# Optimization experiments

Measured on AMD Instinct MI355X. Metric: run time of the kernel, lower is better.

## Reference

```python
import jax, jax.numpy as jnp
import numpy as np
from jax import lax

B, D, N, C = 8, 1, 12288, 256
H = 8            # num_heads
WS = 64          # window size (pixels per window)
HID = 1024       # mlp hidden = 4*C
K = 9            # conv kernel size
EPS = 1e-5


def setup_inputs() -> dict:
    key = jax.random.key(0)
    ks = jax.random.split(key, 8)
    w = lambda i, shape: jax.random.normal(ks[i], shape, jnp.float32) * 0.02
    return {
        "x": jax.random.normal(ks[0], (B, D, N, C), jnp.float32),
        "ln1_g": jnp.ones((C,), jnp.float32),
        "ln1_b": jnp.zeros((C,), jnp.float32),
        "conv_w": w(1, (C, C, K)),            # OIH layout (out_ch, in_ch, k)
        "conv_b": jnp.zeros((C,), jnp.float32),
        "qkv_w": w(2, (C, 3 * C)),            # stored (in, out): y = x @ W + b
        "qkv_b": jnp.zeros((3 * C,), jnp.float32),
        "proj_w": w(3, (C, C)),
        "proj_b": jnp.zeros((C,), jnp.float32),
        "ln2_g": jnp.ones((C,), jnp.float32),
        "ln2_b": jnp.zeros((C,), jnp.float32),
        "fc1_w": w(4, (C, HID)),
        "fc1_b": jnp.zeros((HID,), jnp.float32),
        "fc2_w": w(5, (HID, C)),
        "fc2_b": jnp.zeros((C,), jnp.float32),
    }


def _layernorm(x, g, b):
    mu = jnp.mean(x, axis=-1, keepdims=True)
    var = jnp.mean(jnp.square(x - mu), axis=-1, keepdims=True)
    return (x - mu) * lax.rsqrt(var + EPS) * g + b


def reference(x, ln1_g, ln1_b, conv_w, conv_b, qkv_w, qkv_b,
              proj_w, proj_b, ln2_g, ln2_b, fc1_w, fc1_b, fc2_w, fc2_b):
    shortcut = x                                  # (B, D, N, C)
    h = _layernorm(x, ln1_g, ln1_b)

    # Conv1d over pixel dim N, channels C, same padding
    hc = h.reshape(B * D, N, C).transpose(0, 2, 1)            # (BD, C, N)
    hc = lax.conv_general_dilated(
        hc, conv_w, window_strides=(1,), padding=[((K - 1) // 2, (K - 1) // 2)],
        dimension_numbers=("NCH", "OIH", "NCH"))
    hc = hc + conv_b[None, :, None]
    h = hc.transpose(0, 2, 1).reshape(B, D, N, C)

    # Window partition (no shift): (B*D*N/WS, WS, C)
    win = h.reshape(-1, WS, C)
    hd = C // H
    qkv = (win @ qkv_w + qkv_b).reshape(-1, WS, 3, H, hd)
    q = qkv[:, :, 0].transpose(0, 2, 1, 3)        # (nW, H, WS, hd)
    k = qkv[:, :, 1].transpose(0, 2, 1, 3)
    v = qkv[:, :, 2].transpose(0, 2, 1, 3)
    scale = hd ** (-0.5)
    attn = jnp.einsum("whqd,whkd->whqk", q * scale, k)
    attn = jax.nn.softmax(attn, axis=-1)
    out = jnp.einsum("whqk,whkd->whqd", attn, v)
    out = out.transpose(0, 2, 1, 3).reshape(-1, WS, C)
    out = out @ proj_w + proj_b

    h = out.reshape(B, D, N, C)
    x1 = shortcut + h                             # residual 1
    mlp_in = _layernorm(x1, ln2_g, ln2_b)
    mlp = jax.nn.gelu(mlp_in @ fc1_w + fc1_b, approximate=False) @ fc2_w + fc2_b
    return x1 + mlp                               # residual 2
```

## Files before the change

kernel.cpp:

```cpp
#include <hip/hip_runtime.h>

#define DEVI __device__ __forceinline__

typedef __attribute__((ext_vector_type(4))) float  f32x4;
typedef __attribute__((ext_vector_type(8))) short  s16x8;
typedef __attribute__((ext_vector_type(4))) short  s16x4;
typedef __attribute__((ext_vector_type(8))) __bf16 bf16x8;

constexpr int  Cc  = 256;
constexpr int  Nn  = 12288;
constexpr int  NP  = 12296;
constexpr long TOK = 98304;

DEVI short f2bf(float f) {
  unsigned u = __builtin_bit_cast(unsigned, f);
  u += 0x7fffu + ((u >> 16) & 1u);
  return (short)(u >> 16);
}

DEVI f32x4 MFMA(s16x8 a, s16x8 b, f32x4 c) {
  return __builtin_amdgcn_mfma_f32_16x16x32_bf16(
      __builtin_bit_cast(bf16x8, a), __builtin_bit_cast(bf16x8, b), c, 0, 0, 0);
}

DEVI void gld16(const void* g, void* l) {
  __builtin_amdgcn_global_load_lds(
      (const __attribute__((address_space(1))) void*)g,
      (__attribute__((address_space(3))) void*)l, 16, 0, 0);
}

DEVI void stage_tile(const short* __restrict__ base, long row0, int ld, int k0,
                     short (*dst)[32], int w, int lane) {
#pragma unroll
  for (int c = 0; c < 2; ++c) {
    int s = w * 2 + c;
    const short* g = base + (row0 + s * 16 + (lane >> 2)) * (long)ld + k0 + (lane & 3) * 8;
    gld16(g, &dst[s * 16][0]);
  }
}

__global__ void prep_k(const float* __restrict__ qkv_w, const float* __restrict__ proj_w,
                       const float* __restrict__ fc1_w, const float* __restrict__ fc2_w,
                       const float* __restrict__ conv_w,
                       short* __restrict__ qkvWt, short* __restrict__ projWt,
                       short* __restrict__ fc1Wt, short* __restrict__ fc2Wt,
                       short* __restrict__ convWt, short* __restrict__ hp) {
  int idx = blockIdx.x * 256 + threadIdx.x;
  if (idx < 196608) {
    int o = idx >> 8, i = idx & 255;
    qkvWt[idx] = f2bf(qkv_w[i * 768 + o]);
    return;
  }
  idx -= 196608;
  if (idx < 65536) {
    int o = idx >> 8, i = idx & 255;
    projWt[idx] = f2bf(proj_w[i * 256 + o]);
    return;
  }
  idx -= 65536;
  if (idx < 262144) {
    int o = idx >> 8, i = idx & 255;
    fc1Wt[idx] = f2bf(fc1_w[i * 1024 + o]);
    return;
  }
  idx -= 262144;
  if (idx < 262144) {
    int o = idx >> 10, i = idx & 1023;
    fc2Wt[idx] = f2bf(fc2_w[i * 256 + o]);
    return;
  }
  idx -= 262144;
  if (idx < 589824) {
    int k = idx >> 16, co = (idx >> 8) & 255, ci = idx & 255;
    convWt[idx] = f2bf(conv_w[co * 2304 + ci * 9 + k]);
    return;
  }
  idx -= 589824;
  if (idx < 16384) {
    int b = idx >> 11, rem = idx & 2047;
    int rs = rem >> 8, ch = rem & 255;
    int p = rs < 4 ? rs : 12288 + rs;
    hp[((long)b * NP + p) * 256 + ch] = 0;
  }
}

__global__ __launch_bounds__(256) void ln_k(const float* __restrict__ x,
                                            const float* __restrict__ gw,
                                            const float* __restrict__ bw,
                                            short* __restrict__ out, int pad) {
  const int tid = threadIdx.x, w = tid >> 6, lane = tid & 63;
  const long t = (long)blockIdx.x * 4 + w;
  f32x4 v = *((const f32x4*)(x + t * 256) + lane);
  float s  = v[0] + v[1] + v[2] + v[3];
  float ss = v[0] * v[0] + v[1] * v[1] + v[2] * v[2] + v[3] * v[3];
#pragma unroll
  for (int mk = 1; mk < 64; mk <<= 1) {
    s  += __shfl_xor(s, mk);
    ss += __shfl_xor(ss, mk);
  }
  const float mu   = s * (1.0f / 256.0f);
  const float var  = ss * (1.0f / 256.0f) - mu * mu;
  const float rstd = rsqrtf(var + 1e-5f);
  f32x4 g4 = *((const f32x4*)gw + lane);
  f32x4 b4 = *((const f32x4*)bw + lane);
  const long orow = pad ? (t + (t / Nn) * 8 + 4) : t;
  s16x4 o4;
#pragma unroll
  for (int j = 0; j < 4; ++j) o4[j] = f2bf((v[j] - mu) * rstd * g4[j] + b4[j]);
  *((s16x4*)(out + orow * 256) + lane) = o4;
}

template <int EPI>
__global__ __launch_bounds__(256, 2) void gemm_k(
    const short* __restrict__ A, int lda,
    const short* __restrict__ Bt,
    const float* __restrict__ bias,
    const float* res, short* outS, float* outF,
    int ldo, int K) {
  __shared__ __align__(16) short As[128][32];
  __shared__ __align__(16) short Bs[128][32];
  const int tid = threadIdx.x, w = tid >> 6, lane = tid & 63;
  const int q = lane >> 4, r16 = lane & 15;
  const long row0 = (long)blockIdx.y * 128;
  const int  col0 = blockIdx.x * 128;
  const int  wr = w >> 1, wc = w & 1;
  f32x4 acc[4][4] = {};

  for (int k0 = 0; k0 < K; k0 += 32) {
    stage_tile(A, row0, lda, k0, As, w, lane);
    stage_tile(Bt, col0, K, k0, Bs, w, lane);
    __syncthreads();
    s16x8 af[4], bfv[4];
#pragma unroll
    for (int m = 0; m < 4; ++m) af[m] = *(const s16x8*)&As[wr * 64 + m * 16 + r16][q * 8];
#pragma unroll
    for (int n = 0; n < 4; ++n) bfv[n] = *(const s16x8*)&Bs[wc * 64 + n * 16 + r16][q * 8];
#pragma unroll
    for (int m = 0; m < 4; ++m)
#pragma unroll
      for (int n = 0; n < 4; ++n) acc[m][n] = MFMA(af[m], bfv[n], acc[m][n]);
    __syncthreads();
  }

  const long orow = row0 + wr * 64;
  const int  ocol = col0 + wc * 64;
#pragma unroll
  for (int n = 0; n < 4; ++n) {
    const int   gc = ocol + n * 16 + r16;
    const float bn = bias[gc];
#pragma unroll
    for (int m = 0; m < 4; ++m) {
      const long gr = orow + m * 16 + q * 4;
#pragma unroll
      for (int r = 0; r < 4; ++r) {
        float v = acc[m][n][r] + bn;
        const long o = (gr + r) * (long)ldo + gc;
        if constexpr (EPI == 0) {
          outS[o] = f2bf(v);
        } else if constexpr (EPI == 1) {
          outF[o] = v + res[o];
        } else {
          float t = 0.5f * v * (1.0f + erff(v * 0.70710678118654752f));
          outS[o] = f2bf(t);
        }
      }
    }
  }
}

__global__ __launch_bounds__(256, 2) void conv_k(const short* __restrict__ hp,
                                                 const short* __restrict__ convWt,
                                                 const float* __restrict__ bias,
                                                 short* __restrict__ out) {
  __shared__ __align__(16) short As[128][32];
  __shared__ __align__(16) short Bs[128][32];
  const int tid = threadIdx.x, w = tid >> 6, lane = tid & 63;
  const int q = lane >> 4, r16 = lane & 15;
  const long row0 = (long)blockIdx.y * 128;
  const int  col0 = blockIdx.x * 128;
  const int  b  = (int)(row0 / Nn);
  const int  n0 = (int)(row0 % Nn);
  const long hpbase = (long)b * NP + n0;
  const int  wr = w >> 1, wc = w & 1;
  f32x4 acc[4][4] = {};

  for (int k = 0; k < 9; ++k) {
    const short* Ak = hp + (hpbase + k) * 256;
    const short* Bk = convWt + k * 65536;
    for (int k0 = 0; k0 < 256; k0 += 32) {
      stage_tile(Ak, 0, 256, k0, As, w, lane);
      stage_tile(Bk, col0, 256, k0, Bs, w, lane);
      __syncthreads();
      s16x8 af[4], bfv[4];
#pragma unroll
      for (int m = 0; m < 4; ++m) af[m] = *(const s16x8*)&As[wr * 64 + m * 16 + r16][q * 8];
#pragma unroll
      for (int n = 0; n < 4; ++n) bfv[n] = *(const s16x8*)&Bs[wc * 64 + n * 16 + r16][q * 8];
#pragma unroll
      for (int m = 0; m < 4; ++m)
#pragma unroll
        for (int n = 0; n < 4; ++n) acc[m][n] = MFMA(af[m], bfv[n], acc[m][n]);
      __syncthreads();
    }
  }

  const long orow = row0 + wr * 64;
  const int  ocol = col0 + wc * 64;
#pragma unroll
  for (int n = 0; n < 4; ++n) {
    const int   gc = ocol + n * 16 + r16;
    const float bn = bias[gc];
#pragma unroll
    for (int m = 0; m < 4; ++m) {
      const long gr = orow + m * 16 + q * 4;
#pragma unroll
      for (int r = 0; r < 4; ++r) out[(gr + r) * 256L + gc] = f2bf(acc[m][n][r] + bn);
    }
  }
}

__global__ __launch_bounds__(256, 2) void attn_k(const short* __restrict__ qkv,
                                                 short* __restrict__ o) {
  __shared__ __align__(16) short Pt[4][64][68];
  __shared__ __align__(16) short Vs[4][64][32];
  const int tid = threadIdx.x, w = tid >> 6, lane = tid & 63;
  const int q = lane >> 4, r16 = lane & 15;
  const int job = blockIdx.x * 4 + w;
  const int win = job >> 3, h = job & 7;
  const short* base = qkv + (long)win * 64 * 768;

#pragma unroll
  for (int c = 0; c < 4; ++c) {
    const int idx16 = c * 64 + lane;
    const short* g = base + (long)(idx16 >> 2) * 768 + 512 + h * 32 + (idx16 & 3) * 8;
    gld16(g, (char*)&Vs[w][0][0] + c * 1024);
  }

  s16x8 aq[4], bk[4];
#pragma unroll
  for (int m = 0; m < 4; ++m)
    aq[m] = *(const s16x8*)(base + (long)(m * 16 + r16) * 768 + h * 32 + q * 8);
#pragma unroll
  for (int n = 0; n < 4; ++n)
    bk[n] = *(const s16x8*)(base + (long)(n * 16 + r16) * 768 + 256 + h * 32 + q * 8);
  f32x4 sc[4][4] = {};
#pragma unroll
  for (int m = 0; m < 4; ++m)
#pragma unroll
    for (int n = 0; n < 4; ++n) sc[m][n] = MFMA(aq[m], bk[n], sc[m][n]);

  const float scale = 0.17677669529663687f;
#pragma unroll
  for (int m = 0; m < 4; ++m) {
#pragma unroll
    for (int r = 0; r < 4; ++r) {
      float a0 = sc[m][0][r] * scale, a1 = sc[m][1][r] * scale;
      float a2 = sc[m][2][r] * scale, a3 = sc[m][3][r] * scale;
      float mx = fmaxf(fmaxf(a0, a1), fmaxf(a2, a3));
      mx = fmaxf(mx, __shfl_xor(mx, 1));
      mx = fmaxf(mx, __shfl_xor(mx, 2));
      mx = fmaxf(mx, __shfl_xor(mx, 4));
      mx = fmaxf(mx, __shfl_xor(mx, 8));
      float e0 = __expf(a0 - mx), e1 = __expf(a1 - mx);
      float e2 = __expf(a2 - mx), e3 = __expf(a3 - mx);
      float sm = e0 + e1 + e2 + e3;
      sm += __shfl_xor(sm, 1);
      sm += __shfl_xor(sm, 2);
      sm += __shfl_xor(sm, 4);
      sm += __shfl_xor(sm, 8);
      float inv = 1.0f / sm;
      sc[m][0][r] = e0 * inv; sc[m][1][r] = e1 * inv;
      sc[m][2][r] = e2 * inv; sc[m][3][r] = e3 * inv;
    }
  }

#pragma unroll
  for (int m = 0; m < 4; ++m)
#pragma unroll
    for (int n = 0; n < 4; ++n) {
      s16x4 p4;
#pragma unroll
      for (int r = 0; r < 4; ++r) p4[r] = f2bf(sc[m][n][r]);
      *(s16x4*)&Pt[w][n * 16 + r16][m * 16 + q * 4] = p4;
    }

  asm volatile("s_waitcnt vmcnt(0)" ::: "memory");

  f32x4 oa[4][2] = {};
#pragma unroll
  for (int ks = 0; ks < 2; ++ks) {
    s16x8 bv[2];
#pragma unroll
    for (int nt = 0; nt < 2; ++nt)
#pragma unroll
      for (int jj = 0; jj < 8; ++jj)
        bv[nt][jj] = Vs[w][ks * 32 + q * 8 + jj][nt * 16 + r16];
#pragma unroll
    for (int m = 0; m < 4; ++m) {
      s16x8 ap;
#pragma unroll
      for (int jj = 0; jj < 8; ++jj)
        ap[jj] = Pt[w][ks * 32 + q * 8 + jj][m * 16 + r16];
#pragma unroll
      for (int nt = 0; nt < 2; ++nt) oa[m][nt] = MFMA(ap, bv[nt], oa[m][nt]);
    }
  }

  short* ob = o + (long)win * 64 * 256 + h * 32;
#pragma unroll
  for (int m = 0; m < 4; ++m)
#pragma unroll
    for (int nt = 0; nt < 2; ++nt)
#pragma unroll
      for (int r = 0; r < 4; ++r)
        ob[(long)(m * 16 + q * 4 + r) * 256 + nt * 16 + r16] = f2bf(oa[m][nt][r]);
}

extern "C" void kernel_launch(void* const* d_in, const int* in_sizes, int n_in,
                              void* d_out, int out_size, void* d_ws, size_t ws_size,
                              hipStream_t stream) {
  const float* x      = (const float*)d_in[0];
  const float* ln1_g  = (const float*)d_in[1];
  const float* ln1_b  = (const float*)d_in[2];
  const float* conv_w = (const float*)d_in[3];
  const float* conv_b = (const float*)d_in[4];
  const float* qkv_w  = (const float*)d_in[5];
  const float* qkv_b  = (const float*)d_in[6];
  const float* proj_w = (const float*)d_in[7];
  const float* proj_b = (const float*)d_in[8];
  const float* ln2_g  = (const float*)d_in[9];
  const float* ln2_b  = (const float*)d_in[10];
  const float* fc1_w  = (const float*)d_in[11];
  const float* fc1_b  = (const float*)d_in[12];
  const float* fc2_w  = (const float*)d_in[13];
  const float* fc2_b  = (const float*)d_in[14];
  float* out = (float*)d_out;

  constexpr long HPsz = (long)8 * NP * 256;
  constexpr long Qsz  = TOK * 768;
  constexpr long Csz  = TOK * 256;
  short* ws    = (short*)d_ws;
  short* hp    = ws;
  short* qkvB  = ws + HPsz;
  short* cvB   = ws + HPsz + Qsz;
  short* hidB  = qkvB;
  short* wts   = ws + HPsz + Qsz + Csz;
  short* qkvWt  = wts;
  short* projWt = qkvWt + 196608;
  short* fc1Wt  = projWt + 65536;
  short* fc2Wt  = fc1Wt + 262144;
  short* convWt = fc2Wt + 262144;

  prep_k<<<5440, 256, 0, stream>>>(qkv_w, proj_w, fc1_w, fc2_w, conv_w,
                                   qkvWt, projWt, fc1Wt, fc2Wt, convWt, hp);
  ln_k<<<24576, 256, 0, stream>>>(x, ln1_g, ln1_b, hp, 1);
  conv_k<<<dim3(2, 768), 256, 0, stream>>>(hp, convWt, conv_b, cvB);
  gemm_k<0><<<dim3(6, 768), 256, 0, stream>>>(cvB, 256, qkvWt, qkv_b,
                                              nullptr, qkvB, nullptr, 768, 256);
  attn_k<<<3072, 256, 0, stream>>>(qkvB, hp);
  gemm_k<1><<<dim3(2, 768), 256, 0, stream>>>(hp, 256, projWt, proj_b,
                                              x, nullptr, out, 256, 256);
  ln_k<<<24576, 256, 0, stream>>>(out, ln2_g, ln2_b, hp, 0);
  gemm_k<2><<<dim3(8, 768), 256, 0, stream>>>(hp, 256, fc1Wt, fc1_b,
                                              nullptr, hidB, nullptr, 1024, 256);
  gemm_k<1><<<dim3(2, 768), 256, 0, stream>>>(hidB, 1024, fc2Wt, fc2_b,
                                              out, nullptr, out, 256, 1024);
}
```

Measured before the change: 740.8 us.

## Reuse conv input tile across taps, widen GEMM K-tiles, fuse proj with LN2

Measured after the change: 671.3 us. 9.4% less time.

```diff
diff --git a/kernel.cpp b/kernel.cpp
--- a/kernel.cpp
+++ b/kernel.cpp
@@ -7,7 +7,6 @@
 typedef __attribute__((ext_vector_type(4))) short  s16x4;
 typedef __attribute__((ext_vector_type(8))) __bf16 bf16x8;
 
-constexpr int  Cc  = 256;
 constexpr int  Nn  = 12288;
 constexpr int  NP  = 12296;
 constexpr long TOK = 98304;
@@ -29,14 +28,23 @@
       (__attribute__((address_space(3))) void*)l, 16, 0, 0);
 }
 
-DEVI void stage_tile(const short* __restrict__ base, long row0, int ld, int k0,
-                     short (*dst)[32], int w, int lane) {
-#pragma unroll
-  for (int c = 0; c < 2; ++c) {
-    int s = w * 2 + c;
-    const short* g = base + (row0 + s * 16 + (lane >> 2)) * (long)ld + k0 + (lane & 3) * 8;
-    gld16(g, &dst[s * 16][0]);
-  }
+template <int UNITS>
+DEVI void stage64(const short* __restrict__ g_base, long g_row0, int ld, int k0,
+                  short* __restrict__ lds, int w, int lane) {
+#pragma unroll
+  for (int cc = 0; cc < UNITS; ++cc) {
+    const int u = cc * 256 + w * 64 + lane;
+    const int row = u >> 3, ch = u & 7;
+    const short* g = g_base + (g_row0 + row) * (long)ld + k0 + ch * 8;
+    gld16(g, lds + (cc * 256 + w * 64) * 8);
+  }
+}
+
+DEVI void xcd_decode(int W, int total, int ncol, long& row0, int& col0) {
+  const int per = total >> 3;
+  const int L = (W & 7) * per + (W >> 3);
+  row0 = (long)(L / ncol) * 128;
+  col0 = (L % ncol) * 128;
 }
 
 __global__ void prep_k(const float* __restrict__ qkv_w, const float* __restrict__ proj_w,
@@ -71,7 +79,8 @@
   }
   idx -= 262144;
   if (idx < 589824) {
-    int k = idx >> 16, co = (idx >> 8) & 255, ci = idx & 255;
+    int co = idx / 2304, rem = idx % 2304;
+    int k = rem >> 8, ci = rem & 255;
     convWt[idx] = f2bf(conv_w[co * 2304 + ci * 9 + k]);
     return;
   }
@@ -87,7 +96,7 @@
 __global__ __launch_bounds__(256) void ln_k(const float* __restrict__ x,
                                             const float* __restrict__ gw,
                                             const float* __restrict__ bw,
-                                            short* __restrict__ out, int pad) {
+                                            short* __restrict__ out) {
   const int tid = threadIdx.x, w = tid >> 6, lane = tid & 63;
   const long t = (long)blockIdx.x * 4 + w;
   f32x4 v = *((const f32x4*)(x + t * 256) + lane);
@@ -103,7 +112,7 @@
   const float rstd = rsqrtf(var + 1e-5f);
   f32x4 g4 = *((const f32x4*)gw + lane);
   f32x4 b4 = *((const f32x4*)bw + lane);
-  const long orow = pad ? (t + (t / Nn) * 8 + 4) : t;
+  const long orow = t + (t / Nn) * 8 + 4;
   s16x4 o4;
 #pragma unroll
   for (int j = 0; j < 4; ++j) o4[j] = f2bf((v[j] - mu) * rstd * g4[j] + b4[j]);
@@ -116,29 +125,32 @@
     const short* __restrict__ Bt,
     const float* __restrict__ bias,
     const float* res, short* outS, float* outF,
-    int ldo, int K) {
-  __shared__ __align__(16) short As[128][32];
-  __shared__ __align__(16) short Bs[128][32];
+    int ldo, int K, int ncol) {
+  __shared__ __align__(16) short As[128][64];
+  __shared__ __align__(16) short Bs[128][64];
   const int tid = threadIdx.x, w = tid >> 6, lane = tid & 63;
   const int q = lane >> 4, r16 = lane & 15;
-  const long row0 = (long)blockIdx.y * 128;
-  const int  col0 = blockIdx.x * 128;
-  const int  wr = w >> 1, wc = w & 1;
+  long row0; int col0;
+  xcd_decode(blockIdx.x, gridDim.x, ncol, row0, col0);
+  const int wr = w >> 1, wc = w & 1;
   f32x4 acc[4][4] = {};
 
-  for (int k0 = 0; k0 < K; k0 += 32) {
-    stage_tile(A, row0, lda, k0, As, w, lane);
-    stage_tile(Bt, col0, K, k0, Bs, w, lane);
+  for (int k0 = 0; k0 < K; k0 += 64) {
+    stage64<4>(A, row0, lda, k0, &As[0][0], w, lane);
+    stage64<4>(Bt, col0, K, k0, &Bs[0][0], w, lane);
     __syncthreads();
-    s16x8 af[4], bfv[4];
-#pragma unroll
-    for (int m = 0; m < 4; ++m) af[m] = *(const s16x8*)&As[wr * 64 + m * 16 + r16][q * 8];
-#pragma unroll
-    for (int n = 0; n < 4; ++n) bfv[n] = *(const s16x8*)&Bs[wc * 64 + n * 16 + r16][q * 8];
-#pragma unroll
-    for (int m = 0; m < 4; ++m)
-#pragma unroll
-      for (int n = 0; n < 4; ++n) acc[m][n] = MFMA(af[m], bfv[n], acc[m][n]);
+#pragma unroll
+    for (int kk = 0; kk < 2; ++kk) {
+      s16x8 af[4], bfv[4];
+#pragma unroll
+      for (int m = 0; m < 4; ++m) af[m] = *(const s16x8*)&As[wr * 64 + m * 16 + r16][kk * 32 + q * 8];
+#pragma unroll
+      for (int n = 0; n < 4; ++n) bfv[n] = *(const s16x8*)&Bs[wc * 64 + n * 16 + r16][kk * 32 + q * 8];
+#pragma unroll
+      for (int m = 0; m < 4; ++m)
+#pragma unroll
+        for (int n = 0; n < 4; ++n) acc[m][n] = MFMA(af[m], bfv[n], acc[m][n]);
+    }
     __syncthreads();
   }
 
@@ -172,34 +184,37 @@
                                                  const short* __restrict__ convWt,
                                                  const float* __restrict__ bias,
                                                  short* __restrict__ out) {
-  __shared__ __align__(16) short As[128][32];
-  __shared__ __align__(16) short Bs[128][32];
+  __shared__ __align__(16) short As[160][64];
+  __shared__ __align__(16) short Bs[128][64];
   const int tid = threadIdx.x, w = tid >> 6, lane = tid & 63;
   const int q = lane >> 4, r16 = lane & 15;
-  const long row0 = (long)blockIdx.y * 128;
-  const int  col0 = blockIdx.x * 128;
+  long row0; int col0;
+  xcd_decode(blockIdx.x, gridDim.x, 2, row0, col0);
   const int  b  = (int)(row0 / Nn);
   const int  n0 = (int)(row0 % Nn);
-  const long hpbase = (long)b * NP + n0;
+  const long abase = (long)b * NP + n0;
   const int  wr = w >> 1, wc = w & 1;
   f32x4 acc[4][4] = {};
 
-  for (int k = 0; k < 9; ++k) {
-    const short* Ak = hp + (hpbase + k) * 256;
-    const short* Bk = convWt + k * 65536;
-    for (int k0 = 0; k0 < 256; k0 += 32) {
-      stage_tile(Ak, 0, 256, k0, As, w, lane);
-      stage_tile(Bk, col0, 256, k0, Bs, w, lane);
+  for (int k0 = 0; k0 < 256; k0 += 64) {
+    stage64<5>(hp, abase, 256, k0, &As[0][0], w, lane);
+    for (int tap = 0; tap < 9; ++tap) {
+      stage64<4>(convWt, col0, 2304, tap * 256 + k0, &Bs[0][0], w, lane);
       __syncthreads();
-      s16x8 af[4], bfv[4];
-#pragma unroll
-      for (int m = 0; m < 4; ++m) af[m] = *(const s16x8*)&As[wr * 64 + m * 16 + r16][q * 8];
-#pragma unroll
-      for (int n = 0; n < 4; ++n) bfv[n] = *(const s16x8*)&Bs[wc * 64 + n * 16 + r16][q * 8];
-#pragma unroll
-      for (int m = 0; m < 4; ++m)
-#pragma unroll
-        for (int n = 0; n < 4; ++n) acc[m][n] = MFMA(af[m], bfv[n], acc[m][n]);
+#pragma unroll
+      for (int kk = 0; kk < 2; ++kk) {
+        s16x8 af[4], bfv[4];
+#pragma unroll
+        for (int m = 0; m < 4; ++m)
+          af[m] = *(const s16x8*)&As[tap + wr * 64 + m * 16 + r16][kk * 32 + q * 8];
+#pragma unroll
+        for (int n = 0; n < 4; ++n)
+          bfv[n] = *(const s16x8*)&Bs[wc * 64 + n * 16 + r16][kk * 32 + q * 8];
+#pragma unroll
+        for (int m = 0; m < 4; ++m)
+#pragma unroll
+          for (int n = 0; n < 4; ++n) acc[m][n] = MFMA(af[m], bfv[n], acc[m][n]);
+      }
       __syncthreads();
     }
   }
@@ -217,6 +232,95 @@
       for (int r = 0; r < 4; ++r) out[(gr + r) * 256L + gc] = f2bf(acc[m][n][r] + bn);
     }
   }
+}
+
+__global__ __launch_bounds__(256, 2) void proj_ln_k(
+    const short* __restrict__ A,
+    const short* __restrict__ Bt,
+    const float* __restrict__ bias,
+    const float* __restrict__ res,
+    const float* __restrict__ gw, const float* __restrict__ bw,
+    float* __restrict__ x1,
+    short* __restrict__ lnout) {
+  __shared__ __align__(16) short As[128][64];
+  __shared__ __align__(16) short Bs[256][64];
+  __shared__ float red[2][128][2];
+  const int tid = threadIdx.x, w = tid >> 6, lane = tid & 63;
+  const int q = lane >> 4, r16 = lane & 15;
+  const int W = blockIdx.x, per = gridDim.x >> 3;
+  const long row0 = (long)((W & 7) * per + (W >> 3)) * 128;
+  const int wr = w >> 1, wc = w & 1;
+  f32x4 acc[4][8] = {};
+
+  for (int k0 = 0; k0 < 256; k0 += 64) {
+    stage64<4>(A, row0, 256, k0, &As[0][0], w, lane);
+    stage64<8>(Bt, 0, 256, k0, &Bs[0][0], w, lane);
+    __syncthreads();
+#pragma unroll
+    for (int kk = 0; kk < 2; ++kk) {
+      s16x8 af[4], bfv[8];
+#pragma unroll
+      for (int m = 0; m < 4; ++m) af[m] = *(const s16x8*)&As[wr * 64 + m * 16 + r16][kk * 32 + q * 8];
+#pragma unroll
+      for (int n = 0; n < 8; ++n) bfv[n] = *(const s16x8*)&Bs[wc * 128 + n * 16 + r16][kk * 32 + q * 8];
+#pragma unroll
+      for (int m = 0; m < 4; ++m)
+#pragma unroll
+        for (int n = 0; n < 8; ++n) acc[m][n] = MFMA(af[m], bfv[n], acc[m][n]);
+    }
+    __syncthreads();
+  }
+
+  float s[4][4] = {}, ss[4][4] = {};
+#pragma unroll
+  for (int n = 0; n < 8; ++n) {
+    const int   gc = wc * 128 + n * 16 + r16;
+    const float bn = bias[gc];
+#pragma unroll
+    for (int m = 0; m < 4; ++m) {
+#pragma unroll
+      for (int r = 0; r < 4; ++r) {
+        const long gr = row0 + wr * 64 + m * 16 + q * 4 + r;
+        float v = acc[m][n][r] + bn + res[gr * 256 + gc];
+        acc[m][n][r] = v;
+        x1[gr * 256 + gc] = v;
+        s[m][r] += v;
+        ss[m][r] += v * v;
+      }
+    }
+  }
+#pragma unroll
+  for (int m = 0; m < 4; ++m)
+#pragma unroll
+    for (int r = 0; r < 4; ++r) {
+#pragma unroll
+      for (int mk = 1; mk < 16; mk <<= 1) {
+        s[m][r]  += __shfl_xor(s[m][r], mk);
+        ss[m][r] += __shfl_xor(ss[m][r], mk);
+      }
+      if (r16 == 0) {
+        const int lr = wr * 64 + m * 16 + q * 4 + r;
+        red[wc][lr][0] = s[m][r];
+        red[wc][lr][1] = ss[m][r];
+      }
+    }
+  __syncthreads();
+#pragma unroll
+  for (int m = 0; m < 4; ++m)
+#pragma unroll
+    for (int r = 0; r < 4; ++r) {
+      const int  lr = wr * 64 + m * 16 + q * 4 + r;
+      const long gr = row0 + lr;
+      const float S  = red[0][lr][0] + red[1][lr][0];
+      const float SS = red[0][lr][1] + red[1][lr][1];
+      const float mu = S * (1.0f / 256.0f);
+      const float rstd = rsqrtf(SS * (1.0f / 256.0f) - mu * mu + 1e-5f);
+#pragma unroll
+      for (int n = 0; n < 8; ++n) {
+        const int gc = wc * 128 + n * 16 + r16;
+        lnout[gr * 256 + gc] = f2bf((acc[m][n][r] - mu) * rstd * gw[gc] + bw[gc]);
+      }
+    }
 }
 
 __global__ __launch_bounds__(256, 2) void attn_k(const short* __restrict__ qkv,
@@ -353,16 +457,14 @@
 
   prep_k<<<5440, 256, 0, stream>>>(qkv_w, proj_w, fc1_w, fc2_w, conv_w,
                                    qkvWt, projWt, fc1Wt, fc2Wt, convWt, hp);
-  ln_k<<<24576, 256, 0, stream>>>(x, ln1_g, ln1_b, hp, 1);
-  conv_k<<<dim3(2, 768), 256, 0, stream>>>(hp, convWt, conv_b, cvB);
-  gemm_k<0><<<dim3(6, 768), 256, 0, stream>>>(cvB, 256, qkvWt, qkv_b,
-                                              nullptr, qkvB, nullptr, 768, 256);
+  ln_k<<<24576, 256, 0, stream>>>(x, ln1_g, ln1_b, hp);
+  conv_k<<<1536, 256, 0, stream>>>(hp, convWt, conv_b, cvB);
+  gemm_k<0><<<4608, 256, 0, stream>>>(cvB, 256, qkvWt, qkv_b,
+                                      nullptr, qkvB, nullptr, 768, 256, 6);
   attn_k<<<3072, 256, 0, stream>>>(qkvB, hp);
-  gemm_k<1><<<dim3(2, 768), 256, 0, stream>>>(hp, 256, projWt, proj_b,
-                                              x, nullptr, out, 256, 256);
-  ln_k<<<24576, 256, 0, stream>>>(out, ln2_g, ln2_b, hp, 0);
-  gemm_k<2><<<dim3(8, 768), 256, 0, stream>>>(hp, 256, fc1Wt, fc1_b,
-                                              nullptr, hidB, nullptr, 1024, 256);
-  gemm_k<1><<<dim3(2, 768), 256, 0, stream>>>(hidB, 1024, fc2Wt, fc2_b,
-                                              out, nullptr, out, 256, 1024);
-}
+  proj_ln_k<<<768, 256, 0, stream>>>(hp, projWt, proj_b, x, ln2_g, ln2_b, out, hp);
+  gemm_k<2><<<6144, 256, 0, stream>>>(hp, 256, fc1Wt, fc1_b,
+                                      nullptr, hidB, nullptr, 1024, 256, 8);
+  gemm_k<1><<<1536, 256, 0, stream>>>(hidB, 1024, fc2Wt, fc2_b,
+                                      out, nullptr, out, 256, 1024, 2);
+}
```
